# Kernel tuning notes

Measured on AMD Instinct MI355X. Metric: run time of the kernel, lower is better.

## Reference

```python
import jax, jax.numpy as jnp
import numpy as np

IN_F = 256
OUT_F = 256
ALPHA = 0.01  # LeakyReLU negative slope
NEG_INF = -1e9


def setup_inputs() -> dict:
    key = jax.random.key(0)
    k_inp, k_adj, k_W, k_a = jax.random.split(key, 4)
    inp = jax.random.normal(k_inp, (8, 2048, IN_F), dtype=jnp.float32)
    adj = jax.random.randint(k_adj, (2048, 2048), 0, 2, dtype=jnp.int32)
    # xavier_uniform with gain=1.414
    gain = 1.414
    lim_W = gain * np.sqrt(6.0 / (IN_F + OUT_F))
    W = jax.random.uniform(k_W, (IN_F, OUT_F), minval=-lim_W, maxval=lim_W, dtype=jnp.float32)
    lim_a = gain * np.sqrt(6.0 / (2 * OUT_F + 1))
    a = jax.random.uniform(k_a, (2 * OUT_F, 1), minval=-lim_a, maxval=lim_a, dtype=jnp.float32)
    return {"inp": inp, "adj": adj, "W": W, "a": a}


def reference(inp, adj, W, a):
    # h: [B, N, F]
    h = jnp.matmul(inp, W)
    # Additive attention decomposed: e_ij = leaky_relu(h_i . a1 + h_j . a2)
    # (mathematically identical to concat([h_i, h_j]) @ a, without the O(N^2 * 2F) intermediate)
    a1 = a[:OUT_F, 0]  # [F]
    a2 = a[OUT_F:, 0]  # [F]
    e_src = jnp.einsum('bnf,f->bn', h, a1)  # [B, N]
    e_dst = jnp.einsum('bnf,f->bn', h, a2)  # [B, N]
    e = jax.nn.leaky_relu(e_src[:, :, None] + e_dst[:, None, :], negative_slope=ALPHA)  # [B, N, N]
    e = jnp.where(adj[None, :, :] == 0, NEG_INF, e)
    attention = jax.nn.softmax(e, axis=-1)
    # dropout is identity in eval mode
    h_prime = jnp.matmul(attention, h)  # [B, N, F]
    return jax.nn.relu(h_prime)  # concat=True path
```

## Files before the change

kernel.cpp:

```cpp
#include <hip/hip_runtime.h>
#include <hip/hip_bf16.h>
#include <stdint.h>

#define N_NODES 2048
#define FDIM 256

typedef short bf16x8 __attribute__((ext_vector_type(8)));
typedef float f32x4 __attribute__((ext_vector_type(4)));
typedef unsigned short u16x4 __attribute__((ext_vector_type(4)));

static __device__ __forceinline__ unsigned short bf16r(float x) {
  __hip_bfloat16 h = __float2bfloat16(x);
  return __builtin_bit_cast(unsigned short, h);
}

__global__ __launch_bounds__(256) void k_prep(const float* __restrict__ W, const float* __restrict__ a,
                                              __hip_bfloat16* __restrict__ WT16,
                                              float* __restrict__ wa1, float* __restrict__ wa2) {
  int bid = blockIdx.x, t = threadIdx.x;
  if (bid < 16) {
    __shared__ __hip_bfloat16 T[64][67];
    int k0 = (bid & 3) * 64, f0 = (bid >> 2) * 64;
    int r = t >> 2, c0 = (t & 3) * 16;
    #pragma unroll
    for (int i = 0; i < 4; ++i) {
      f32x4 v = *(const f32x4*)(W + (size_t)(k0 + r) * FDIM + f0 + c0 + i * 4);
      #pragma unroll
      for (int j = 0; j < 4; ++j) T[r][c0 + i * 4 + j] = __float2bfloat16(v[j]);
    }
    __syncthreads();
    int fr = t >> 2, kc = (t & 3) * 16;
    unsigned short buf[16];
    #pragma unroll
    for (int i = 0; i < 16; ++i) buf[i] = __builtin_bit_cast(unsigned short, T[kc + i][fr]);
    uint4* dst = (uint4*)(WT16 + (size_t)(f0 + fr) * FDIM + k0 + kc);
    dst[0] = *(uint4*)&buf[0];
    dst[1] = *(uint4*)&buf[8];
  } else {
    int k = (bid - 16) * 64 + (t >> 2), q = t & 3;
    float s1 = 0.f, s2 = 0.f;
    #pragma unroll
    for (int i = 0; i < 16; ++i) {
      int f = q * 64 + i * 4;
      f32x4 w  = *(const f32x4*)(W + (size_t)k * FDIM + f);
      f32x4 v1 = *(const f32x4*)(a + f);
      f32x4 v2 = *(const f32x4*)(a + FDIM + f);
      #pragma unroll
      for (int j = 0; j < 4; ++j) { s1 += w[j] * v1[j]; s2 += w[j] * v2[j]; }
    }
    s1 += __shfl_xor(s1, 1); s1 += __shfl_xor(s1, 2);
    s2 += __shfl_xor(s2, 1); s2 += __shfl_xor(s2, 2);
    if (q == 0) { wa1[k] = s1; wa2[k] = s2; }
  }
}

__global__ __launch_bounds__(256) void k_h2p(const float* __restrict__ inp,
                                             const int* __restrict__ adj, uint32_t* __restrict__ adjp,
                                             const __hip_bfloat16* __restrict__ WT16,
                                             const float* __restrict__ wa1, const float* __restrict__ wa2,
                                             __hip_bfloat16* __restrict__ Bf,
                                             float* __restrict__ e_src, float* __restrict__ e_dst) {
  __shared__ char lds_raw[20480];
  __hip_bfloat16* Asm = (__hip_bfloat16*)lds_raw;
  int t = threadIdx.x;
  int r0 = blockIdx.x * 32;
  int b = r0 >> 11, j0 = r0 & (N_NODES - 1);

  {
    int prow = blockIdx.x * 4 + (t >> 6);
    int lane = t & 63;
    const int* row = adj + (size_t)prow * N_NODES;
    #pragma unroll
    for (int it = 0; it < 32; ++it) {
      int v = row[it * 64 + lane];
      unsigned long long m = __ballot(v != 0);
      if (lane == 0) {
        adjp[prow * 64 + it * 2]     = (uint32_t)(m & 0xffffffffull);
        adjp[prow * 64 + it * 2 + 1] = (uint32_t)(m >> 32);
      }
    }
  }

  {
    int r = t >> 3, q = t & 7, c0 = q * 32;
    const float* ip = inp + (size_t)(r0 + r) * FDIM + c0;
    float s1 = 0.f, s2 = 0.f;
    #pragma unroll
    for (int i = 0; i < 8; ++i) {
      f32x4 v  = *(const f32x4*)(ip + i * 4);
      f32x4 u1 = *(const f32x4*)(wa1 + c0 + i * 4);
      f32x4 u2 = *(const f32x4*)(wa2 + c0 + i * 4);
      u16x4 pk;
      #pragma unroll
      for (int j = 0; j < 4; ++j) {
        s1 += v[j] * u1[j];
        s2 += v[j] * u2[j];
        pk[j] = bf16r(v[j]);
      }
      *(u16x4*)(Asm + r * 264 + c0 + i * 4) = pk;
    }
    s1 += __shfl_xor(s1, 1); s1 += __shfl_xor(s1, 2); s1 += __shfl_xor(s1, 4);
    s2 += __shfl_xor(s2, 1); s2 += __shfl_xor(s2, 2); s2 += __shfl_xor(s2, 4);
    if (q == 0) { e_src[r0 + r] = s1; e_dst[r0 + r] = s2; }
  }
  __syncthreads();

  int lane = t & 63, wv = t >> 6, l15 = lane & 15, lq = lane >> 4;
  int f0 = wv * 64;
  f32x4 acc[2][4];
  #pragma unroll
  for (int mf = 0; mf < 2; ++mf)
    #pragma unroll
    for (int nf = 0; nf < 4; ++nf)
      #pragma unroll
      for (int e = 0; e < 4; ++e) acc[mf][nf][e] = 0.f;

  #pragma unroll
  for (int ks = 0; ks < 8; ++ks) {
    int k0 = ks * 32;
    bf16x8 af[2], bfr[4];
    #pragma unroll
    for (int mf = 0; mf < 2; ++mf)
      af[mf] = *(const bf16x8*)(Asm + (mf * 16 + l15) * 264 + k0 + lq * 8);
    #pragma unroll
    for (int nf = 0; nf < 4; ++nf)
      bfr[nf] = *(const bf16x8*)(WT16 + (size_t)(f0 + nf * 16 + l15) * FDIM + k0 + lq * 8);
    #pragma unroll
    for (int mf = 0; mf < 2; ++mf)
      #pragma unroll
      for (int nf = 0; nf < 4; ++nf)
        acc[mf][nf] = __builtin_amdgcn_mfma_f32_16x16x32_bf16(af[mf], bfr[nf], acc[mf][nf], 0, 0, 0);
  }

  __syncthreads();
  __hip_bfloat16* Tsm = (__hip_bfloat16*)lds_raw;
  #pragma unroll
  for (int mf = 0; mf < 2; ++mf)
    #pragma unroll
    for (int nf = 0; nf < 4; ++nf) {
      u16x4 pk;
      #pragma unroll
      for (int r = 0; r < 4; ++r) pk[r] = bf16r(acc[mf][nf][r]);
      int fl = f0 + nf * 16 + l15;
      int jl = mf * 16 + lq * 4;
      *(u16x4*)(Tsm + fl * 40 + jl) = pk;
    }
  __syncthreads();
  {
    int kt = j0 >> 5;
    #pragma unroll
    for (int q = 0; q < 4; ++q) {
      int ft = (t >> 6) * 4 + q;
      uint4 v = *(const uint4*)(Tsm + (ft * 16 + l15) * 40 + lq * 8);
      *(uint4*)(Bf + ((((size_t)b * 16 + ft) * 64 + kt) * 64 + lane) * 8) = v;
    }
  }
}

__global__ __launch_bounds__(512) void k_pvF4(const __hip_bfloat16* __restrict__ Bf,
                                              const uint32_t* __restrict__ adjp,
                                              const float* __restrict__ e_src,
                                              const float* __restrict__ e_dst,
                                              float* __restrict__ out) {
  __shared__ __align__(16) char Abuf[32768];
  __shared__ float sm_ed[2048];
  __shared__ uint32_t sm_adj[64 * 65];
  __shared__ float sm_es[64], sm_m[64], sm_il[64];
  int t = threadIdx.x;
  int b  = blockIdx.x & 7;
  int it = blockIdx.x >> 3;
  int i0 = it * 64;
  int lane = t & 63, wv = t >> 6, l15 = lane & 15, lq = lane >> 4;
  int sub = wv & 3, par = wv >> 2;

  *(f32x4*)(sm_ed + t * 4) = *(const f32x4*)(e_dst + ((size_t)b << 11) + t * 4);
  {
    int row = t >> 3, q = t & 7;
    const uint4* s = (const uint4*)(adjp + (size_t)(i0 + row) * 64 + q * 8);
    uint32_t* d = sm_adj + row * 65 + q * 8;
    uint4 v0 = s[0], v1 = s[1];
    *(uint4*)(d) = v0; *(uint4*)(d + 4) = v1;
  }
  __syncthreads();

  for (int rr = 0; rr < 8; ++rr) {
    int iloc = wv * 8 + rr;
    float es = e_src[(b << 11) + i0 + iloc];
    float ev[32];
    float mx = -3e38f;
    #pragma unroll
    for (int c = 0; c < 32; ++c) {
      int j = c * 64 + lane;
      float s = es + sm_ed[j];
      float lr = fmaxf(s, 0.01f * s);
      uint32_t w = sm_adj[iloc * 65 + (j >> 5)];
      float e = ((w >> (j & 31)) & 1u) ? lr : -1e9f;
      ev[c] = e;
      mx = fmaxf(mx, e);
    }
    #pragma unroll
    for (int m = 1; m <= 32; m <<= 1) mx = fmaxf(mx, __shfl_xor(mx, m));
    float sum = 0.f;
    #pragma unroll
    for (int c = 0; c < 32; ++c) sum += __expf(ev[c] - mx);
    #pragma unroll
    for (int m = 1; m <= 32; m <<= 1) sum += __shfl_xor(sum, m);
    if (lane == 0) { sm_es[iloc] = es; sm_m[iloc] = mx; sm_il[iloc] = 1.0f / sum; }
  }
  __syncthreads();

  int fr_row = sub * 16 + l15;
  float es = sm_es[fr_row], mi = sm_m[fr_row], ili = sm_il[fr_row];
  int adjbase = fr_row * 65;
  int edoff = lq * 8;

  auto computeA = [&](int k0) -> uint4 {
    uint32_t w = sm_adj[adjbase + k0] >> (lq * 8);
    f32x4 e0 = *(const f32x4*)(sm_ed + k0 * 32 + edoff);
    f32x4 e1 = *(const f32x4*)(sm_ed + k0 * 32 + edoff + 4);
    unsigned short u[8];
    #pragma unroll
    for (int e = 0; e < 8; ++e) {
      float ed = (e < 4) ? e0[e] : e1[e - 4];
      float s = es + ed;
      float lr = fmaxf(s, 0.01f * s);
      float p = __expf(lr - mi) * ili;
      p = ((w >> e) & 1u) ? p : 0.0f;
      u[e] = bf16r(p);
    }
    uint4 v;
    v.x = (uint32_t)u[0] | ((uint32_t)u[1] << 16);
    v.y = (uint32_t)u[2] | ((uint32_t)u[3] << 16);
    v.z = (uint32_t)u[4] | ((uint32_t)u[5] << 16);
    v.w = (uint32_t)u[6] | ((uint32_t)u[7] << 16);
    return v;
  };

  auto produce = [&](int buf, int ch) {
    #pragma unroll
    for (int q = 0; q < 2; ++q) {
      int k0l = q * 2 + par;
      uint4 fr = computeA(ch * 4 + k0l);
      *(uint4*)(Abuf + (((buf * 4 + k0l) * 4 + sub) << 10) + lane * 16) = fr;
    }
  };

  const __hip_bfloat16* Bp0 = Bf + (((size_t)b * 16 + wv * 2)     * 64) * 512 + (size_t)lane * 8;
  const __hip_bfloat16* Bp1 = Bf + (((size_t)b * 16 + wv * 2 + 1) * 64) * 512 + (size_t)lane * 8;

  f32x4 acc[4][2];
  #pragma unroll
  for (int m = 0; m < 4; ++m)
    #pragma unroll
    for (int n = 0; n < 2; ++n)
      #pragma unroll
      for (int e = 0; e < 4; ++e) acc[m][n][e] = 0.f;

  bf16x8 bA0 = *(const bf16x8*)(Bp0);
  bf16x8 bA1 = *(const bf16x8*)(Bp1);
  bf16x8 bB0 = *(const bf16x8*)(Bp0 + 512);
  bf16x8 bB1 = *(const bf16x8*)(Bp1 + 512);

  produce(0, 0);
  __syncthreads();

  for (int ch = 0; ch < 16; ++ch) {
    int buf = ch & 1;
    if (ch < 15) produce(buf ^ 1, ch + 1);
    const char* Ab = Abuf + buf * 16384;
    #pragma unroll
    for (int k0l = 0; k0l < 4; ++k0l) {
      int k0 = ch * 4 + k0l;
      bf16x8 af[4];
      #pragma unroll
      for (int m = 0; m < 4; ++m)
        af[m] = *(const bf16x8*)(Ab + ((k0l * 4 + m) << 10) + lane * 16);
      bf16x8 cb0 = (k0l & 1) ? bB0 : bA0;
      bf16x8 cb1 = (k0l & 1) ? bB1 : bA1;
      if (k0 + 2 < 64) {
        if (k0l & 1) { bB0 = *(const bf16x8*)(Bp0 + (size_t)(k0 + 2) * 512); bB1 = *(const bf16x8*)(Bp1 + (size_t)(k0 + 2) * 512); }
        else         { bA0 = *(const bf16x8*)(Bp0 + (size_t)(k0 + 2) * 512); bA1 = *(const bf16x8*)(Bp1 + (size_t)(k0 + 2) * 512); }
      }
      #pragma unroll
      for (int m = 0; m < 4; ++m) {
        acc[m][0] = __builtin_amdgcn_mfma_f32_16x16x32_bf16(af[m], cb0, acc[m][0], 0, 0, 0);
        acc[m][1] = __builtin_amdgcn_mfma_f32_16x16x32_bf16(af[m], cb1, acc[m][1], 0, 0, 0);
      }
    }
    __syncthreads();
  }

  #pragma unroll
  for (int m = 0; m < 4; ++m)
    #pragma unroll
    for (int n = 0; n < 2; ++n) {
      int col = (wv * 2 + n) * 16 + l15;
      int orow = (b << 11) + i0 + m * 16 + lq * 4;
      #pragma unroll
      for (int r = 0; r < 4; ++r)
        out[(size_t)(orow + r) * FDIM + col] = fmaxf(acc[m][n][r], 0.0f);
    }
}

extern "C" void kernel_launch(void* const* d_in, const int* in_sizes, int n_in,
                              void* d_out, int out_size, void* d_ws, size_t ws_size,
                              hipStream_t stream) {
  const float* inp = (const float*)d_in[0];
  const int*   adj = (const int*)d_in[1];
  const float* W   = (const float*)d_in[2];
  const float* a   = (const float*)d_in[3];
  float* out = (float*)d_out;
  char* ws = (char*)d_ws;

  __hip_bfloat16* Bf   = (__hip_bfloat16*)ws;
  float* e_src         = (float*)(ws + 8388608);
  float* e_dst         = (float*)(ws + 8454144);
  __hip_bfloat16* WT16 = (__hip_bfloat16*)(ws + 8519680);
  float* wa1           = (float*)(ws + 8650752);
  float* wa2           = (float*)(ws + 8651776);
  uint32_t* adjp       = (uint32_t*)(ws + 8652800);

  k_prep<<<20, 256, 0, stream>>>(W, a, WT16, wa1, wa2);
  k_h2p<<<512, 256, 0, stream>>>(inp, adj, adjp, WT16, wa1, wa2, Bf, e_src, e_dst);
  k_pvF4<<<256, 512, 0, stream>>>(Bf, adjp, e_src, e_dst, out);
}
```

Measured before the change: 81.99 us.

## Split softmax row statistics into separate log-sum-exp kernel using base-2 exponentials

Moves the per-row max and sum computation out of the attention-times-V kernel into a new kernel that writes one log-sum-exp value per row. It also folds log2(e) into the attention projection weights, so every exponential becomes a hardware exp2 and the normalisation turns into a subtraction inside the exponent. The goal is to shorten the serial softmax prologue in the main kernel, which runs on only 256 blocks, and to cut the ALU work per probability element. In exchange it adds a kernel launch and an extra global read of e_dst and adjacency per row. LeakyReLU commutes with a positive scale, so scaling e_src and e_dst by log2(e) keeps the result exact.

```diff
diff --git a/kernel.cpp b/kernel.cpp
--- a/kernel.cpp
+++ b/kernel.cpp
@@ -4,6 +4,7 @@
 
 #define N_NODES 2048
 #define FDIM 256
+#define LOG2E 1.44269504088896340736f
 
 typedef short bf16x8 __attribute__((ext_vector_type(8)));
 typedef float f32x4 __attribute__((ext_vector_type(4)));
@@ -13,6 +14,9 @@
   __hip_bfloat16 h = __float2bfloat16(x);
   return __builtin_bit_cast(unsigned short, h);
 }
+
+static __device__ __forceinline__ float exp2_hw(float x) { return __builtin_amdgcn_exp2f(x); }
+static __device__ __forceinline__ float log2_hw(float x) { return __builtin_amdgcn_logf(x); }
 
 __global__ __launch_bounds__(256) void k_prep(const float* __restrict__ W, const float* __restrict__ a,
                                               __hip_bfloat16* __restrict__ WT16,
@@ -50,7 +54,7 @@
     }
     s1 += __shfl_xor(s1, 1); s1 += __shfl_xor(s1, 2);
     s2 += __shfl_xor(s2, 1); s2 += __shfl_xor(s2, 2);
-    if (q == 0) { wa1[k] = s1; wa2[k] = s2; }
+    if (q == 0) { wa1[k] = s1 * LOG2E; wa2[k] = s2 * LOG2E; }
   }
 }
 
@@ -157,15 +161,49 @@
   }
 }
 
-__global__ __launch_bounds__(512) void k_pvF4(const __hip_bfloat16* __restrict__ Bf,
-                                              const uint32_t* __restrict__ adjp,
-                                              const float* __restrict__ e_src,
-                                              const float* __restrict__ e_dst,
-                                              float* __restrict__ out) {
+__global__ __launch_bounds__(256) void k_lse(const uint32_t* __restrict__ adjp,
+                                             const float* __restrict__ e_src,
+                                             const float* __restrict__ e_dst,
+                                             float* __restrict__ lserow) {
+  int t = threadIdx.x;
+  int lane = t & 63;
+  int r = blockIdx.x * 4 + (t >> 6);
+  int b = r >> 11, i = r & (N_NODES - 1);
+  float es = e_src[r];
+  const float* edb = e_dst + ((size_t)b << 11);
+  const uint32_t* arow = adjp + (size_t)i * 64;
+  float ev[32];
+  float mx = -3e38f;
+  #pragma unroll
+  for (int it = 0; it < 32; ++it) {
+    int j = it * 64 + lane;
+    float ed = edb[j];
+    uint32_t w = arow[j >> 5];
+    float s = es + ed;
+    float lr = fmaxf(s, 0.01f * s);
+    float e = ((w >> (j & 31)) & 1u) ? lr : -1e9f;
+    ev[it] = e;
+    mx = fmaxf(mx, e);
+  }
+  #pragma unroll
+  for (int m = 1; m <= 32; m <<= 1) mx = fmaxf(mx, __shfl_xor(mx, m));
+  float sum = 0.f;
+  #pragma unroll
+  for (int it = 0; it < 32; ++it) sum += exp2_hw(ev[it] - mx);
+  #pragma unroll
+  for (int m = 1; m <= 32; m <<= 1) sum += __shfl_xor(sum, m);
+  if (lane == 0) lserow[r] = mx + log2_hw(sum);
+}
+
+__global__ __launch_bounds__(512) void k_pvF3L(const __hip_bfloat16* __restrict__ Bf,
+                                               const uint32_t* __restrict__ adjp,
+                                               const float* __restrict__ e_src,
+                                               const float* __restrict__ e_dst,
+                                               const float* __restrict__ lserow,
+                                               float* __restrict__ out) {
   __shared__ __align__(16) char Abuf[32768];
   __shared__ float sm_ed[2048];
   __shared__ uint32_t sm_adj[64 * 65];
-  __shared__ float sm_es[64], sm_m[64], sm_il[64];
   int t = threadIdx.x;
   int b  = blockIdx.x & 7;
   int it = blockIdx.x >> 3;
@@ -181,38 +219,13 @@
     uint4 v0 = s[0], v1 = s[1];
     *(uint4*)(d) = v0; *(uint4*)(d + 4) = v1;
   }
-  __syncthreads();
-
-  for (int rr = 0; rr < 8; ++rr) {
-    int iloc = wv * 8 + rr;
-    float es = e_src[(b << 11) + i0 + iloc];
-    float ev[32];
-    float mx = -3e38f;
-    #pragma unroll
-    for (int c = 0; c < 32; ++c) {
-      int j = c * 64 + lane;
-      float s = es + sm_ed[j];
-      float lr = fmaxf(s, 0.01f * s);
-      uint32_t w = sm_adj[iloc * 65 + (j >> 5)];
-      float e = ((w >> (j & 31)) & 1u) ? lr : -1e9f;
-      ev[c] = e;
-      mx = fmaxf(mx, e);
-    }
-    #pragma unroll
-    for (int m = 1; m <= 32; m <<= 1) mx = fmaxf(mx, __shfl_xor(mx, m));
-    float sum = 0.f;
-    #pragma unroll
-    for (int c = 0; c < 32; ++c) sum += __expf(ev[c] - mx);
-    #pragma unroll
-    for (int m = 1; m <= 32; m <<= 1) sum += __shfl_xor(sum, m);
-    if (lane == 0) { sm_es[iloc] = es; sm_m[iloc] = mx; sm_il[iloc] = 1.0f / sum; }
-  }
-  __syncthreads();
-
-  int fr_row = sub * 16 + l15;
-  float es = sm_es[fr_row], mi = sm_m[fr_row], ili = sm_il[fr_row];
-  int adjbase = fr_row * 65;
+  int rg = (b << 11) + i0 + sub * 16 + l15;
+  float es = e_src[rg], lse = lserow[rg];
+  float esl = es - lse;
+  float c2  = fmaf(0.01f, es, -lse);
+  int adjbase = (sub * 16 + l15) * 65;
   int edoff = lq * 8;
+  __syncthreads();
 
   auto computeA = [&](int k0) -> uint4 {
     uint32_t w = sm_adj[adjbase + k0] >> (lq * 8);
@@ -222,9 +235,8 @@
     #pragma unroll
     for (int e = 0; e < 8; ++e) {
       float ed = (e < 4) ? e0[e] : e1[e - 4];
-      float s = es + ed;
-      float lr = fmaxf(s, 0.01f * s);
-      float p = __expf(lr - mi) * ili;
+      float v = fmaxf(esl + ed, fmaf(0.01f, ed, c2));
+      float p = exp2_hw(v);
       p = ((w >> e) & 1u) ? p : 0.0f;
       u[e] = bf16r(p);
     }
@@ -315,12 +327,14 @@
   __hip_bfloat16* Bf   = (__hip_bfloat16*)ws;
   float* e_src         = (float*)(ws + 8388608);
   float* e_dst         = (float*)(ws + 8454144);
-  __hip_bfloat16* WT16 = (__hip_bfloat16*)(ws + 8519680);
-  float* wa1           = (float*)(ws + 8650752);
-  float* wa2           = (float*)(ws + 8651776);
-  uint32_t* adjp       = (uint32_t*)(ws + 8652800);
+  float* lserow        = (float*)(ws + 8519680);
+  __hip_bfloat16* WT16 = (__hip_bfloat16*)(ws + 8585216);
+  float* wa1           = (float*)(ws + 8716288);
+  float* wa2           = (float*)(ws + 8717312);
+  uint32_t* adjp       = (uint32_t*)(ws + 8718336);
 
   k_prep<<<20, 256, 0, stream>>>(W, a, WT16, wa1, wa2);
   k_h2p<<<512, 256, 0, stream>>>(inp, adj, adjp, WT16, wa1, wa2, Bf, e_src, e_dst);
-  k_pvF4<<<256, 512, 0, stream>>>(Bf, adjp, e_src, e_dst, out);
-}
+  k_lse<<<4096, 256, 0, stream>>>(adjp, e_src, e_dst, lserow);
+  k_pvF3L<<<256, 512, 0, stream>>>(Bf, adjp, e_src, e_dst, lserow, out);
+}
```

Result: faster. 79.45 us (-3.1%).
